# Kernel tuning notes

Measured on AMD Instinct MI355X. Metric: run time of the kernel, lower is better.

Reference implementation:

```python
import jax, jax.numpy as jnp
import numpy as np

PAD = 7                 # init padding
T = 2 * PAD + 1         # T_side_dense = 15 shifts per axis
LAMDA = 1.0             # init lamda
EPS = 1e-16             # hardcoded epsilon in the torch loss body


def _joint_hist(x_out, x_tf_out):
    # Equivalent of F.conv2d(x_out.permute(1,0,2,3), weight=x_tf_out.permute(1,0,2,3), padding=PAD)
    # expressed as T*T shifted matmuls (correlation / cost-volume form).
    bn, k, h, w = x_out.shape
    A = jnp.transpose(x_out, (1, 0, 2, 3))      # (k, bn, h, w)  conv "input"
    B = jnp.transpose(x_tf_out, (1, 0, 2, 3))   # (k, bn, h, w)  conv "weight"
    A_pad = jnp.pad(A, ((0, 0), (0, 0), (PAD, PAD), (PAD, PAD)))

    def step(carry, s):
        dy, dx = s // T, s % T
        sl = jax.lax.dynamic_slice(A_pad, (0, 0, dy, dx), (k, bn, h, w))
        # p[n, o] at this shift = sum_{c,y,x} A_pad[n,c,y+dy,x+dx] * B[o,c,y,x]
        return carry, jnp.einsum('nchw,ochw->no', sl, B)

    _, p = jax.lax.scan(step, None, jnp.arange(T * T))
    # (T*T, k, k) -> (T, T, k, k); matches torch p_i_j.permute(2, 3, 0, 1)
    return p.reshape(T, T, k, k)


def reference(x_out, x_tf_out):
    p = _joint_hist(x_out, x_tf_out)
    # shift to positive; min is detached in torch -> stop_gradient
    p = p - jax.lax.stop_gradient(p.min()) + EPS
    # normalize per shift over the (k, k) joint
    p = p / p.sum(axis=(2, 3), keepdims=True)
    # symmetrize
    p = (p + jnp.swapaxes(p, 2, 3)) / 2.0
    p_i = p.sum(axis=2, keepdims=True)   # (T, T, 1, k) marginal (broadcasts like repeat)
    p_j = p.sum(axis=3, keepdims=True)   # (T, T, k, 1) marginal
    loss = (-p * (jnp.log(p + EPS)
                  - LAMDA * jnp.log(p_i + EPS)
                  - LAMDA * jnp.log(p_j + EPS))).sum() / (T * T)
    return loss


def setup_inputs() -> dict:
    key = jax.random.key(0)
    k1, k2 = jax.random.split(key)
    bn, k, h, w = 16, 10, 224, 224
    # simplex over axis=1 is asserted by the torch module -> use softmax
    x_out = jax.nn.softmax(jax.random.normal(k1, (bn, k, h, w), dtype=jnp.float32), axis=1)
    x_tf_out = jax.nn.softmax(jax.random.normal(k2, (bn, k, h, w), dtype=jnp.float32), axis=1)
    return {"x_out": x_out, "x_tf_out": x_tf_out}
```

## Files before the change

### kernel.cpp

```cpp
#include <hip/hip_runtime.h>
#include <stdint.h>
#include <math.h>


#define PADV 7
#define TS 15
#define KCLS 10
#define HH 224
#define WW 224
#define MD 160
#define NCELL (MD*MD)
#define NBLK 256
#define TY 14
#define BSTRIDE 232
#define BPH 240
#define ADW 120
#define LEPS 1e-16

typedef __attribute__((ext_vector_type(4))) float f32x4;
typedef __attribute__((ext_vector_type(8))) short bf16x8;

__device__ __forceinline__ unsigned short f2bf(float f) {
  union { float f; uint32_t u; } v; v.f = f;
  return (unsigned short)((v.u + 0x7FFFu + ((v.u >> 16) & 1u)) >> 16);
}

__device__ __forceinline__ void glds16(const unsigned short* g, unsigned short* l) {
  __builtin_amdgcn_global_load_lds(
      (const __attribute__((address_space(1))) unsigned int*)g,
      (__attribute__((address_space(3))) unsigned int*)l, 16, 0, 0);
}

struct U5 { uint32_t u[5]; };

__device__ __forceinline__ void ldA5(const uint32_t* p, U5& d) {
  uint4 t;
  __builtin_memcpy(&t, p, 16);
  d.u[0] = t.x; d.u[1] = t.y; d.u[2] = t.z; d.u[3] = t.w;
  d.u[4] = p[4];
}

#define BPREP_BLOCKS 4350
#define APREP_BLOCKS 4200
__global__ __launch_bounds__(256)
void prep(const float* __restrict__ xo, const float* __restrict__ xt,
          unsigned short* __restrict__ bp, uint32_t* __restrict__ ap) {
  if (blockIdx.x < BPREP_BLOCKS) {
    const int idx   = blockIdx.x * 256 + threadIdx.x;
    const int rowid = idx / 29;
    const int chunk = idx - rowid * 29;
    const int x0    = chunk * 8;
    const int yy    = rowid % BPH;
    const int cls   = rowid / BPH;
    const int row   = yy - PADV;
    union { unsigned short h[8]; uint4 v; } out;
    if (row >= 0 && row < HH && x0 < WW) {
      const float* src = xt + ((size_t)cls * HH + row) * WW + x0;
#pragma unroll
      for (int j = 0; j < 8; ++j) out.h[j] = f2bf(src[j]);
    } else {
      out.v = make_uint4(0u, 0u, 0u, 0u);
    }
    *(uint4*)(bp + (size_t)rowid * BSTRIDE + x0) = out.v;
  } else {
    const int idx   = (blockIdx.x - BPREP_BLOCKS) * 256 + threadIdx.x;
    const int rowid = idx / 30;
    const int wg    = idx - rowid * 30;
    const float* src = xo + (size_t)rowid * WW;
    float e[8];
#pragma unroll
    for (int j = 0; j < 8; ++j) {
      const int x = 8 * wg + j - PADV;
      e[j] = (x >= 0 && x < WW) ? src[x] : 0.f;
    }
    union { uint32_t u[4]; uint4 v; } o;
#pragma unroll
    for (int k = 0; k < 4; ++k)
      o.u[k] = (uint32_t)f2bf(e[2 * k]) | ((uint32_t)f2bf(e[2 * k + 1]) << 16);
    *(uint4*)(ap + (size_t)rowid * ADW + 4 * wg) = o.v;
  }
}

__global__ __launch_bounds__(512, 1)
void corr_gemm(const uint32_t* __restrict__ apad,
               const unsigned short* __restrict__ bpad,
               float* __restrict__ partials) {
  __shared__ __align__(16) unsigned short ldsB[KCLS * 16 * BSTRIDE];

  const int tid  = threadIdx.x;
  const int bid  = blockIdx.x;
  const int b    = bid >> 4;
  const int y0   = (bid & 15) * TY;

  const int lane = tid & 63;
  const int wv   = tid >> 6;
  const int wm   = wv & 1;
  const int wn   = (wv >> 1) & 1;
  const int kw   = wv >> 2;
  const int quad = lane >> 4;
  const int l15  = lane & 15;

  const int shA    = (l15 & 1) << 4;
  const int laneWd = quad * 4 + (l15 >> 1);

  f32x4 acc[5][5];
#pragma unroll
  for (int i = 0; i < 5; ++i)
#pragma unroll
    for (int j = 0; j < 5; ++j) acc[i][j] = (f32x4){0.f, 0.f, 0.f, 0.f};

  const unsigned short* Bb = bpad + (size_t)b * KCLS * BPH * BSTRIDE;
  const uint32_t* Abase = apad + ((size_t)(b * KCLS + wm * 5) * HH) * ADW;

  for (int pr = wv; pr < 15 * KCLS; pr += 8) {
    const int r15  = pr / KCLS;
    const int o    = pr - r15 * KCLS;
    const int yy   = y0 + r15;
    const int slot = (y0 - PADV + r15) & 15;
    if (lane < 29)
      glds16(Bb + ((size_t)o * BPH + yy) * BSTRIDE + lane * 8,
             ldsB + (o * 16 + slot) * BSTRIDE);
  }

  U5 bufA[5], bufB[5];
#pragma unroll
  for (int mi = 0; mi < 5; ++mi)
    ldA5(Abase + ((size_t)mi * HH + y0) * ADW + kw * 16 + laneWd, bufA[mi]);

  __syncthreads();

  auto stepf = [&](int y, int xc, U5 (&use)[5], U5 (&pre)[5],
                   int pny, int pnxc, bool dopre) {
    if (dopre) {
#pragma unroll
      for (int mi = 0; mi < 5; ++mi)
        ldA5(Abase + ((size_t)mi * HH + pny) * ADW + pnxc * 16 + laneWd, pre[mi]);
    }
    bf16x8 afrag[5];
#pragma unroll
    for (int mi = 0; mi < 5; ++mi) {
      union { uint32_t u[4]; bf16x8 v; } cv;
      cv.u[0] = __builtin_amdgcn_alignbit(use[mi].u[1], use[mi].u[0], shA);
      cv.u[1] = __builtin_amdgcn_alignbit(use[mi].u[2], use[mi].u[1], shA);
      cv.u[2] = __builtin_amdgcn_alignbit(use[mi].u[3], use[mi].u[2], shA);
      cv.u[3] = __builtin_amdgcn_alignbit(use[mi].u[4], use[mi].u[3], shA);
      afrag[mi] = cv.v;
    }
    const int x0    = xc * 32;
    const int slotB = (y + PADV - l15) & 15;
    bf16x8 bfrag[5];
#pragma unroll
    for (int ni = 0; ni < 5; ++ni) {
      const int to = wn * 5 + ni;
      bfrag[ni] = *(const bf16x8*)(ldsB + (to * 16 + slotB) * BSTRIDE + x0 + quad * 8);
    }
#pragma unroll
    for (int mi = 0; mi < 5; ++mi)
#pragma unroll
      for (int ni = 0; ni < 5; ++ni)
        acc[mi][ni] = __builtin_amdgcn_mfma_f32_16x16x32_bf16(
            afrag[mi], bfrag[ni], acc[mi][ni], 0, 0, 0);
  };

  auto dmaB = [&](int y) {
    const int yy   = y + 15;
    const int slot = (y + 8) & 15;
    for (int ro = wv - 4; ro < KCLS; ro += 4)
      if (lane < 29)
        glds16(Bb + ((size_t)ro * BPH + yy) * BSTRIDE + lane * 8,
               ldsB + (ro * 16 + slot) * BSTRIDE);
  };

  if (kw == 0) {
#pragma unroll 1
    for (int iy = 0; iy < TY; ++iy) {
      const int y = y0 + iy;
      const bool lastY = (iy == TY - 1);
      stepf(y, 0, bufA, bufB, y, 2, true);
      stepf(y, 2, bufB, bufA, y, 4, true);
      stepf(y, 4, bufA, bufB, y, 6, true);
      stepf(y, 6, bufB, bufA, y + 1, 0, !lastY);
      if (!lastY) __syncthreads();
    }
  } else {
#pragma unroll 1
    for (int iy2 = 0; iy2 < TY; iy2 += 2) {
      {
        const int y = y0 + iy2;
        dmaB(y);
        stepf(y, 1, bufA, bufB, y, 3, true);
        stepf(y, 3, bufB, bufA, y, 5, true);
        stepf(y, 5, bufA, bufB, y + 1, 1, true);
        __syncthreads();
      }
      {
        const int iy = iy2 + 1;
        const int y  = y0 + iy;
        const bool lastY = (iy == TY - 1);
        if (!lastY) dmaB(y);
        stepf(y, 1, bufB, bufA, y, 3, true);
        stepf(y, 3, bufA, bufB, y, 5, true);
        stepf(y, 5, bufB, bufA, y + 1, 1, !lastY);
        if (!lastY) __syncthreads();
      }
    }
  }

  __syncthreads();
  float* ex = (float*)ldsB;
  const int w1 = wm * 2 + wn;
  float* outp = partials + (size_t)bid * NCELL;
#pragma unroll
  for (int rd = 0; rd < 2; ++rd) {
    const int mib = (rd == 0) ? 0 : 3;
    const int nmi = (rd == 0) ? 3 : 2;
    if (kw == 1) {
#pragma unroll
      for (int dmi = 0; dmi < 3; ++dmi) {
        if (dmi >= nmi) break;
#pragma unroll
        for (int ni = 0; ni < 5; ++ni)
          *(f32x4*)(ex + (((w1 * 3 + dmi) * 5 + ni) << 8) + lane * 4) =
              acc[mib + dmi][ni];
      }
    }
    __syncthreads();
    if (kw == 0) {
#pragma unroll
      for (int dmi = 0; dmi < 3; ++dmi) {
        if (dmi >= nmi) break;
        const int mi = mib + dmi;
#pragma unroll
        for (int ni = 0; ni < 5; ++ni) {
          const f32x4 other = *(const f32x4*)(ex + (((w1 * 3 + dmi) * 5 + ni) << 8) + lane * 4);
          const int mrow = (wm * 5 + mi) * 16 + quad * 4;
          const int ncol = (wn * 5 + ni) * 16 + l15;
#pragma unroll
          for (int r = 0; r < 4; ++r)
            outp[(size_t)(mrow + r) * MD + ncol] = acc[mi][ni][r] + other[r];
        }
      }
    }
    __syncthreads();
  }
}

__global__ __launch_bounds__(256)
void reduce_all(const float* __restrict__ partials, float* __restrict__ Cout,
                float* __restrict__ mins, float* __restrict__ dout) {
  const int blk = blockIdx.x;
  const int t   = threadIdx.x;
  const int c   = blk * 64 + (t & 63);
  const int ps  = t >> 6;
  if (blk == 0 && t == 0) dout[0] = 0.f;
  double s0 = 0.0, s1 = 0.0;
  const float* base = partials + c;
  for (int p = ps * 64; p < ps * 64 + 64; p += 2) {
    s0 += (double)base[(size_t)p * NCELL];
    s1 += (double)base[(size_t)(p + 1) * NCELL];
  }
  __shared__ double red[256];
  red[t] = s0 + s1;
  __syncthreads();
  if (t < 64) {
    const double tot = red[t] + red[t + 64] + red[t + 128] + red[t + 192];
    const float sf = (float)tot;
    Cout[c] = sf;
    const int m  = c / MD;
    const int nn = c - m * MD;
    const bool valid = ((m & 15) < TS) && ((nn & 15) < TS);
    float v = valid ? sf : 3.4e38f;
#pragma unroll
    for (int off = 32; off > 0; off >>= 1)
      v = fminf(v, __shfl_down(v, off));
    if (t == 0) mins[blk] = v;
  }
}

__global__ __launch_bounds__(128)
void loss_kernel(const float* __restrict__ Cmat, const float* __restrict__ mins,
                 float* __restrict__ dout) {
  const int s   = blockIdx.x;
  const int dy  = s / TS;
  const int dx  = s - dy * TS;
  const int tid = threadIdx.x;
  __shared__ float fm[128];
  __shared__ double q[100];
  __shared__ double sym[100];
  __shared__ double pi[10], pj[10];
  __shared__ double red[128];

  float v = 3.4e38f;
  for (int i = tid; i < 400; i += 128) v = fminf(v, mins[i]);
  fm[tid] = v;
  __syncthreads();
  for (int st = 64; st > 0; st >>= 1) {
    if (tid < st) fm[tid] = fminf(fm[tid], fm[tid + st]);
    __syncthreads();
  }
  const double minv = (double)fm[0];
  __syncthreads();

  if (tid < 100) {
    const int n = tid / 10, o = tid - (tid / 10) * 10;
    const double vv = (double)Cmat[(size_t)(n * 16 + dx) * MD + (o * 16 + dy)];
    q[tid] = vv - minv + LEPS;
  }
  __syncthreads();
  red[tid] = (tid < 100) ? q[tid] : 0.0;
  __syncthreads();
  for (int st = 64; st > 0; st >>= 1) {
    if (tid < st) red[tid] += red[tid + st];
    __syncthreads();
  }
  const double Z = red[0];
  __syncthreads();
  if (tid < 100) {
    const int n = tid / 10, o = tid - (tid / 10) * 10;
    sym[tid] = (q[n * 10 + o] + q[o * 10 + n]) * 0.5 / Z;
  }
  __syncthreads();
  if (tid < 10) {
    double a = 0.0, bsum = 0.0;
    for (int n2 = 0; n2 < 10; ++n2) {
      a    += sym[n2 * 10 + tid];
      bsum += sym[tid * 10 + n2];
    }
    pi[tid] = a;
    pj[tid] = bsum;
  }
  __syncthreads();
  double term = 0.0;
  if (tid < 100) {
    const int n = tid / 10, o = tid - (tid / 10) * 10;
    const double sp = sym[tid];
    term = -sp * (log(sp + LEPS) - log(pi[o] + LEPS) - log(pj[n] + LEPS));
  }
  red[tid] = term;
  __syncthreads();
  for (int st = 64; st > 0; st >>= 1) {
    if (tid < st) red[tid] += red[tid + st];
    __syncthreads();
  }
  if (tid == 0) atomicAdd(dout, (float)(red[0] / (double)(TS * TS)));
}

extern "C" void kernel_launch(void* const* d_in, const int* in_sizes, int n_in,
                              void* d_out, int out_size, void* d_ws, size_t ws_size,
                              hipStream_t stream) {
  const float* xo = (const float*)d_in[0];
  const float* xt = (const float*)d_in[1];
  float* ws       = (float*)d_ws;

  float* partials = ws;
  float* Cmat     = partials + (size_t)NBLK * NCELL;
  float* mins     = Cmat + NCELL;
  unsigned short* bpad = (unsigned short*)(mins + 512);
  uint32_t* apad  = (uint32_t*)(bpad + (size_t)160 * BPH * BSTRIDE);
  float* out      = (float*)d_out;

  hipLaunchKernelGGL(prep,       dim3(BPREP_BLOCKS + APREP_BLOCKS), dim3(256), 0, stream,
                     xo, xt, bpad, apad);
  hipLaunchKernelGGL(corr_gemm,  dim3(256), dim3(512), 0, stream, apad, bpad, partials);
  hipLaunchKernelGGL(reduce_all, dim3(400), dim3(256), 0, stream, partials, Cmat, mins, out);
  hipLaunchKernelGGL(loss_kernel,dim3(225), dim3(128), 0, stream, Cmat, mins, out);
}
```

Baseline: 166.4 us.

## Load B fragments directly from global memory instead of staging rows in LDS

Removes the LDS ring buffer for B and its per-row DMA and barriers. Each wave now fetches A and B fragments straight from global memory into registers with double buffering. The K split also changes from x-chunks to alternating rows. LDS use shrinks to a small exchange buffer for the final cross-wave reduction, and the launch bound is raised to allow two blocks per CU. The cost is more global/L2 traffic for B and higher register pressure under the tighter occupancy target.

```diff
diff --git a/kernel.cpp b/kernel.cpp
--- a/kernel.cpp
+++ b/kernel.cpp
@@ -11,7 +11,6 @@
 #define MD 160
 #define NCELL (MD*MD)
 #define NBLK 256
-#define TY 14
 #define BSTRIDE 232
 #define BPH 240
 #define ADW 120
@@ -25,20 +24,7 @@
   return (unsigned short)((v.u + 0x7FFFu + ((v.u >> 16) & 1u)) >> 16);
 }
 
-__device__ __forceinline__ void glds16(const unsigned short* g, unsigned short* l) {
-  __builtin_amdgcn_global_load_lds(
-      (const __attribute__((address_space(1))) unsigned int*)g,
-      (__attribute__((address_space(3))) unsigned int*)l, 16, 0, 0);
-}
-
 struct U5 { uint32_t u[5]; };
-
-__device__ __forceinline__ void ldA5(const uint32_t* p, U5& d) {
-  uint4 t;
-  __builtin_memcpy(&t, p, 16);
-  d.u[0] = t.x; d.u[1] = t.y; d.u[2] = t.z; d.u[3] = t.w;
-  d.u[4] = p[4];
-}
 
 #define BPREP_BLOCKS 4350
 #define APREP_BLOCKS 4200
@@ -81,16 +67,16 @@
   }
 }
 
-__global__ __launch_bounds__(512, 1)
+__global__ __launch_bounds__(512, 2)
 void corr_gemm(const uint32_t* __restrict__ apad,
                const unsigned short* __restrict__ bpad,
                float* __restrict__ partials) {
-  __shared__ __align__(16) unsigned short ldsB[KCLS * 16 * BSTRIDE];
+  __shared__ __align__(16) float ex[5120];
 
   const int tid  = threadIdx.x;
   const int bid  = blockIdx.x;
   const int b    = bid >> 4;
-  const int y0   = (bid & 15) * TY;
+  const int y0   = (bid & 15) * 14;
 
   const int lane = tid & 63;
   const int wv   = tid >> 6;
@@ -99,9 +85,21 @@
   const int kw   = wv >> 2;
   const int quad = lane >> 4;
   const int l15  = lane & 15;
-
-  const int shA    = (l15 & 1) << 4;
-  const int laneWd = quad * 4 + (l15 >> 1);
+  const int shA  = (l15 & 1) << 4;
+
+  const int clsA0 = __builtin_amdgcn_readfirstlane(b * KCLS + wm * 5);
+  const int clsB0 = __builtin_amdgcn_readfirstlane(b * KCLS + wn * 5);
+  const char* sA[5];
+  const char* sB[5];
+#pragma unroll
+  for (int mi = 0; mi < 5; ++mi)
+    sA[mi] = (const char*)apad + (size_t)(clsA0 + mi) * HH * (ADW * 4);
+#pragma unroll
+  for (int ni = 0; ni < 5; ++ni)
+    sB[ni] = (const char*)bpad + (size_t)(clsB0 + ni) * BPH * (BSTRIDE * 2) - 4096;
+
+  unsigned voffA = (unsigned)((y0 + kw) * (ADW * 4) + quad * 16 + (l15 >> 1) * 4);
+  unsigned voffB = (unsigned)((y0 + kw + 14 - l15) * (BSTRIDE * 2) + quad * 16 + 4096);
 
   f32x4 acc[5][5];
 #pragma unroll
@@ -109,50 +107,39 @@
 #pragma unroll
     for (int j = 0; j < 5; ++j) acc[i][j] = (f32x4){0.f, 0.f, 0.f, 0.f};
 
-  const unsigned short* Bb = bpad + (size_t)b * KCLS * BPH * BSTRIDE;
-  const uint32_t* Abase = apad + ((size_t)(b * KCLS + wm * 5) * HH) * ADW;
-
-  for (int pr = wv; pr < 15 * KCLS; pr += 8) {
-    const int r15  = pr / KCLS;
-    const int o    = pr - r15 * KCLS;
-    const int yy   = y0 + r15;
-    const int slot = (y0 - PADV + r15) & 15;
-    if (lane < 29)
-      glds16(Bb + ((size_t)o * BPH + yy) * BSTRIDE + lane * 8,
-             ldsB + (o * 16 + slot) * BSTRIDE);
-  }
-
-  U5 bufA[5], bufB[5];
-#pragma unroll
-  for (int mi = 0; mi < 5; ++mi)
-    ldA5(Abase + ((size_t)mi * HH + y0) * ADW + kw * 16 + laneWd, bufA[mi]);
-
-  __syncthreads();
-
-  auto stepf = [&](int y, int xc, U5 (&use)[5], U5 (&pre)[5],
-                   int pny, int pnxc, bool dopre) {
-    if (dopre) {
-#pragma unroll
-      for (int mi = 0; mi < 5; ++mi)
-        ldA5(Abase + ((size_t)mi * HH + pny) * ADW + pnxc * 16 + laneWd, pre[mi]);
-    }
-    bf16x8 afrag[5];
+  U5   curA[5], nxtA[5];
+  uint4 curB[5], nxtB[5];
+
+  auto fetch = [&](int imm, U5 (&A)[5], uint4 (&B)[5]) {
+#pragma unroll
+    for (int mi = 0; mi < 5; ++mi) {
+      uint4 t;
+      __builtin_memcpy(&t, sA[mi] + voffA + imm, 16);
+      A[mi].u[0] = t.x; A[mi].u[1] = t.y; A[mi].u[2] = t.z; A[mi].u[3] = t.w;
+      uint32_t e;
+      __builtin_memcpy(&e, sA[mi] + voffA + imm + 16, 4);
+      A[mi].u[4] = e;
+    }
+#pragma unroll
+    for (int ni = 0; ni < 5; ++ni)
+      __builtin_memcpy(&B[ni], sB[ni] + voffB + imm, 16);
+  };
+
+  auto compute = [&](U5 (&A)[5], uint4 (&B)[5]) {
+    bf16x8 afrag[5], bfrag[5];
 #pragma unroll
     for (int mi = 0; mi < 5; ++mi) {
       union { uint32_t u[4]; bf16x8 v; } cv;
-      cv.u[0] = __builtin_amdgcn_alignbit(use[mi].u[1], use[mi].u[0], shA);
-      cv.u[1] = __builtin_amdgcn_alignbit(use[mi].u[2], use[mi].u[1], shA);
-      cv.u[2] = __builtin_amdgcn_alignbit(use[mi].u[3], use[mi].u[2], shA);
-      cv.u[3] = __builtin_amdgcn_alignbit(use[mi].u[4], use[mi].u[3], shA);
+      cv.u[0] = __builtin_amdgcn_alignbit(A[mi].u[1], A[mi].u[0], shA);
+      cv.u[1] = __builtin_amdgcn_alignbit(A[mi].u[2], A[mi].u[1], shA);
+      cv.u[2] = __builtin_amdgcn_alignbit(A[mi].u[3], A[mi].u[2], shA);
+      cv.u[3] = __builtin_amdgcn_alignbit(A[mi].u[4], A[mi].u[3], shA);
       afrag[mi] = cv.v;
     }
-    const int x0    = xc * 32;
-    const int slotB = (y + PADV - l15) & 15;
-    bf16x8 bfrag[5];
 #pragma unroll
     for (int ni = 0; ni < 5; ++ni) {
-      const int to = wn * 5 + ni;
-      bfrag[ni] = *(const bf16x8*)(ldsB + (to * 16 + slotB) * BSTRIDE + x0 + quad * 8);
+      union { uint4 q; bf16x8 v; } bv; bv.q = B[ni];
+      bfrag[ni] = bv.v;
     }
 #pragma unroll
     for (int mi = 0; mi < 5; ++mi)
@@ -162,86 +149,52 @@
             afrag[mi], bfrag[ni], acc[mi][ni], 0, 0, 0);
   };
 
-  auto dmaB = [&](int y) {
-    const int yy   = y + 15;
-    const int slot = (y + 8) & 15;
-    for (int ro = wv - 4; ro < KCLS; ro += 4)
-      if (lane < 29)
-        glds16(Bb + ((size_t)ro * BPH + yy) * BSTRIDE + lane * 8,
-               ldsB + (ro * 16 + slot) * BSTRIDE);
-  };
-
-  if (kw == 0) {
+  fetch(0, curA, curB);
+
 #pragma unroll 1
-    for (int iy = 0; iy < TY; ++iy) {
-      const int y = y0 + iy;
-      const bool lastY = (iy == TY - 1);
-      stepf(y, 0, bufA, bufB, y, 2, true);
-      stepf(y, 2, bufB, bufA, y, 4, true);
-      stepf(y, 4, bufA, bufB, y, 6, true);
-      stepf(y, 6, bufB, bufA, y + 1, 0, !lastY);
-      if (!lastY) __syncthreads();
-    }
-  } else {
-#pragma unroll 1
-    for (int iy2 = 0; iy2 < TY; iy2 += 2) {
-      {
-        const int y = y0 + iy2;
-        dmaB(y);
-        stepf(y, 1, bufA, bufB, y, 3, true);
-        stepf(y, 3, bufB, bufA, y, 5, true);
-        stepf(y, 5, bufA, bufB, y + 1, 1, true);
-        __syncthreads();
-      }
-      {
-        const int iy = iy2 + 1;
-        const int y  = y0 + iy;
-        const bool lastY = (iy == TY - 1);
-        if (!lastY) dmaB(y);
-        stepf(y, 1, bufB, bufA, y, 3, true);
-        stepf(y, 3, bufA, bufB, y, 5, true);
-        stepf(y, 5, bufB, bufA, y + 1, 1, !lastY);
-        if (!lastY) __syncthreads();
-      }
-    }
-  }
-
-  __syncthreads();
-  float* ex = (float*)ldsB;
+  for (int iy = 0; iy < 7; ++iy) {
+    fetch(64,  nxtA, nxtB);  compute(curA, curB);
+    fetch(128, curA, curB);  compute(nxtA, nxtB);
+    fetch(192, nxtA, nxtB);  compute(curA, curB);
+    fetch(256, curA, curB);  compute(nxtA, nxtB);
+    fetch(320, nxtA, nxtB);  compute(curA, curB);
+    fetch(384, curA, curB);  compute(nxtA, nxtB);
+    voffA += 2 * ADW * 4;
+    voffB += 2 * BSTRIDE * 2;
+    if (iy < 6) fetch(0, nxtA, nxtB);
+    compute(curA, curB);
+    if (iy < 6) {
+#pragma unroll
+      for (int mi = 0; mi < 5; ++mi)
+#pragma unroll
+        for (int r = 0; r < 5; ++r) curA[mi].u[r] = nxtA[mi].u[r];
+#pragma unroll
+      for (int ni = 0; ni < 5; ++ni) curB[ni] = nxtB[ni];
+    }
+  }
+
   const int w1 = wm * 2 + wn;
   float* outp = partials + (size_t)bid * NCELL;
-#pragma unroll
-  for (int rd = 0; rd < 2; ++rd) {
-    const int mib = (rd == 0) ? 0 : 3;
-    const int nmi = (rd == 0) ? 3 : 2;
+#pragma unroll 1
+  for (int r = 0; r < 5; ++r) {
+    __syncthreads();
     if (kw == 1) {
 #pragma unroll
-      for (int dmi = 0; dmi < 3; ++dmi) {
-        if (dmi >= nmi) break;
-#pragma unroll
-        for (int ni = 0; ni < 5; ++ni)
-          *(f32x4*)(ex + (((w1 * 3 + dmi) * 5 + ni) << 8) + lane * 4) =
-              acc[mib + dmi][ni];
+      for (int ni = 0; ni < 5; ++ni)
+        *(f32x4*)(ex + ((w1 * 5 + ni) * 64 + lane) * 4) = acc[r][ni];
+    }
+    __syncthreads();
+    if (kw == 0) {
+      const int mrow = (wm * 5 + r) * 16 + quad * 4;
+#pragma unroll
+      for (int ni = 0; ni < 5; ++ni) {
+        const f32x4 other = *(const f32x4*)(ex + ((w1 * 5 + ni) * 64 + lane) * 4);
+        const int ncol = (wn * 5 + ni) * 16 + l15;
+#pragma unroll
+        for (int rr = 0; rr < 4; ++rr)
+          outp[(size_t)(mrow + rr) * MD + ncol] = acc[r][ni][rr] + other[rr];
       }
     }
-    __syncthreads();
-    if (kw == 0) {
-#pragma unroll
-      for (int dmi = 0; dmi < 3; ++dmi) {
-        if (dmi >= nmi) break;
-        const int mi = mib + dmi;
-#pragma unroll
-        for (int ni = 0; ni < 5; ++ni) {
-          const f32x4 other = *(const f32x4*)(ex + (((w1 * 3 + dmi) * 5 + ni) << 8) + lane * 4);
-          const int mrow = (wm * 5 + mi) * 16 + quad * 4;
-          const int ncol = (wn * 5 + ni) * 16 + l15;
-#pragma unroll
-          for (int r = 0; r < 4; ++r)
-            outp[(size_t)(mrow + r) * MD + ncol] = acc[mi][ni][r] + other[r];
-        }
-      }
-    }
-    __syncthreads();
   }
 }
 
```

After: 218.9 us. 31.6% more time.
